# Kernel tuning notes

Hardware: AMD Instinct MI355X
Metric: run time of the kernel (lower is better)

The kernel has to match this reference:

```python
import jax, jax.numpy as jnp
import numpy as np

B, D, L = 4, 256, 4096

def setup_inputs() -> dict:
    key = jax.random.key(0)
    k1, k2, k3 = jax.random.split(key, 3)
    query = jax.random.normal(k1, (B, D, L), dtype=jnp.float32)
    context = jax.random.normal(k2, (B, D, L), dtype=jnp.float32)
    W_in = jax.random.normal(k3, (D, D), dtype=jnp.float32) * 0.02
    b_in = jnp.zeros((D,), dtype=jnp.float32)
    return {"query": query, "context": context, "W_in": W_in, "b_in": b_in}

def reference(query, context, W_in, b_in):
    # inputs are [B, D, L]; module transposes to [B, L, D]
    q = jnp.transpose(query, (0, 2, 1))    # [B, O, D]
    c = jnp.transpose(context, (0, 2, 1))  # [B, Q, D]
    # 'general': linear_in applied to query only (torch Linear: x @ W^T + b)
    q = q @ W_in.T + b_in
    # unscaled Luong attention: QK^T -> softmax -> A V
    scores = jnp.einsum('bod,bqd->boq', q, c)          # [B, O, Q]
    weights = jax.nn.softmax(scores, axis=-1)          # [B, O, Q]
    out = jnp.einsum('boq,bqd->bod', weights, c)       # [B, O, D]
    return (out, weights)
```

## Files before the change

kernel.cpp:

```cpp
#include <hip/hip_runtime.h>


#define BATCH 4
#define DDIM  256
#define LSEQ  4096
#define TQ    64

typedef float    f32x4 __attribute__((ext_vector_type(4)));
typedef _Float16 f16x8 __attribute__((ext_vector_type(8)));
typedef _Float16 f16x4 __attribute__((ext_vector_type(4)));

__device__ __forceinline__ void gld16(const void* g, void* l) {
  __builtin_amdgcn_global_load_lds((const __attribute__((address_space(1))) void*)g,
                                   (__attribute__((address_space(3))) void*)l, 16, 0, 0);
}

__global__ __launch_bounds__(256) void transpose_cast(
    const float* __restrict__ q_in, const float* __restrict__ c_in,
    _Float16* __restrict__ q_out, _Float16* __restrict__ c_out,
    _Float16* __restrict__ cD16)
{
  __shared__ float tile[64][68];
  const int which = blockIdx.z >> 2;
  const int b     = blockIdx.z & 3;
  const float* __restrict__ src = which ? c_in : q_in;
  _Float16* __restrict__ dst    = which ? c_out : q_out;
  const int l0 = blockIdx.x * 64, d0 = blockIdx.y * 64;
  const int tid = threadIdx.x;
  const int tr = tid >> 4, tc = (tid & 15) << 2;
#pragma unroll
  for (int i = 0; i < 4; ++i) {
    int d = tr + i * 16;
    f32x4 v = *(const f32x4*)(src + ((size_t)b * DDIM + d0 + d) * LSEQ + l0 + tc);
    *(f32x4*)&tile[d][tc] = v;
    if (which) {
      f16x4 h;
      h[0] = (_Float16)v[0]; h[1] = (_Float16)v[1];
      h[2] = (_Float16)v[2]; h[3] = (_Float16)v[3];
      *(f16x4*)(cD16 + ((size_t)b * DDIM + d0 + d) * LSEQ + l0 + tc) = h;
    }
  }
  __syncthreads();
#pragma unroll
  for (int i = 0; i < 4; ++i) {
    int l = tr + i * 16;
    f16x4 h;
    h[0] = (_Float16)tile[tc + 0][l];
    h[1] = (_Float16)tile[tc + 1][l];
    h[2] = (_Float16)tile[tc + 2][l];
    h[3] = (_Float16)tile[tc + 3][l];
    *(f16x4*)(dst + ((size_t)b * LSEQ + l0 + l) * DDIM + d0 + tc) = h;
  }
}

__global__ __launch_bounds__(256) void wconv(const float* __restrict__ w,
                                             _Float16* __restrict__ w16) {
  int i = (blockIdx.x * 256 + threadIdx.x) * 4;
  f32x4 v = *(const f32x4*)(w + i);
  f16x4 h;
  h[0] = (_Float16)v[0]; h[1] = (_Float16)v[1];
  h[2] = (_Float16)v[2]; h[3] = (_Float16)v[3];
  *(f16x4*)(w16 + i) = h;
}

__global__ __launch_bounds__(256) void linear_q(
    const _Float16* __restrict__ qT16, const _Float16* __restrict__ W16,
    const float* __restrict__ bias, _Float16* __restrict__ qw16)
{
  const int tid = threadIdx.x;
  const int wv = tid >> 6, ln = tid & 63, g = ln >> 4, c16 = ln & 15;
  const size_t r0 = (size_t)blockIdx.x * 64 + wv * 16;

  f16x8 qa[8];
  const _Float16* qrow = qT16 + (r0 + c16) * DDIM + g * 8;
#pragma unroll
  for (int kk = 0; kk < 8; ++kk) qa[kk] = *(const f16x8*)(qrow + kk * 32);

  f32x4 acc[16];
#pragma unroll
  for (int n = 0; n < 16; ++n) acc[n] = f32x4{0.f, 0.f, 0.f, 0.f};

#pragma unroll 2
  for (int kk = 0; kk < 8; ++kk) {
#pragma unroll
    for (int n = 0; n < 16; ++n) {
      f16x8 bf = *(const f16x8*)(W16 + (n * 16 + c16) * DDIM + kk * 32 + g * 8);
      acc[n] = __builtin_amdgcn_mfma_f32_16x16x32_f16(qa[kk], bf, acc[n], 0, 0, 0);
    }
  }
#pragma unroll
  for (int n = 0; n < 16; ++n) {
    float bb = bias[n * 16 + c16];
#pragma unroll
    for (int r = 0; r < 4; ++r)
      qw16[(r0 + 4 * g + r) * DDIM + n * 16 + c16] = (_Float16)(acc[n][r] + bb);
  }
}

__global__ __launch_bounds__(1024, 4) void attn_main(
    const _Float16* __restrict__ qw16,
    const _Float16* __restrict__ cT16,
    const _Float16* __restrict__ cD16,
    float* __restrict__ outp,
    float* __restrict__ wgt)
{
  __shared__ __align__(16) char smem[2][32768];
  __shared__ __align__(16) char wbuf[8192];
  __shared__ float redbuf[4][64];
  char* obuf = &smem[0][0];

  const int tid = threadIdx.x;
  const int wv  = tid >> 6;
  const int qw  = wv & 3;
  const int ow  = wv >> 2;
  const int kh  = wv & 1;
  const int dw  = wv >> 1;
  const int ln  = tid & 63;
  const int g   = ln >> 4;
  const int c16 = ln & 15;

  const int lin   = blockIdx.y * 64 + blockIdx.x;
  const int b     = (lin & 7) >> 1;
  const int otile = ((lin >> 3) << 1) | (lin & 1);
  const int o0    = otile * 64;
  const int bo    = b * LSEQ + o0;

  const _Float16* __restrict__ cbase = cT16 + (size_t)b * LSEQ * DDIM;
  const _Float16* __restrict__ cDb   = cD16 + (size_t)b * DDIM * LSEQ;

  f16x8 qb[8];
#pragma unroll
  for (int kk = 0; kk < 8; ++kk)
    qb[kk] = *(const f16x8*)(qw16 +
        ((size_t)(bo + ow * 16 + c16) << 8) + kk * 32 + g * 8);

  auto issue_dma = [&](int t, int pp) {
#pragma unroll
    for (int i = 0; i < 2; ++i) {
      unsigned x  = (unsigned)tid * 16 + i * 16384;
      unsigned q  = x >> 9;
      unsigned db = (x & 511u) ^ ((q & 7u) << 4);
      gld16(cbase + ((size_t)(t * TQ + q) << 8) + (db >> 1), &smem[pp][x]);
    }
  };

  float lsum = 0.f;
  int p = 0;
  issue_dma(0, 0);
  for (int t = 0; t < LSEQ / TQ; ++t) {
    asm volatile("s_waitcnt vmcnt(0)" ::: "memory");
    __builtin_amdgcn_s_barrier();
    issue_dma(t < LSEQ / TQ - 1 ? t + 1 : 0, p ^ 1);
    __builtin_amdgcn_sched_barrier(0);

    const char* cl = smem[p];
    f32x4 sa{0.f, 0.f, 0.f, 0.f};
#pragma unroll
    for (int kk = 0; kk < 8; ++kk) {
      unsigned off = (unsigned)((qw * 16 + c16) * 512 + kk * 64 + g * 16) ^
                     ((unsigned)(c16 & 7) << 4);
      f16x8 af = *(const f16x8*)(cl + off);
      sa = __builtin_amdgcn_mfma_f32_16x16x32_f16(af, qb[kk], sa, 0, 0, 0);
    }
#pragma unroll
    for (int r = 0; r < 4; ++r) lsum += __expf(sa[r]);
    p ^= 1;
  }

  lsum += __shfl_xor(lsum, 16);
  lsum += __shfl_xor(lsum, 32);
  if (ln < 16) redbuf[qw][ow * 16 + ln] = lsum;
  __syncthreads();
  const int o_mine = ow * 16 + c16;
  const float invl = 1.0f / (redbuf[0][o_mine] + redbuf[1][o_mine] +
                             redbuf[2][o_mine] + redbuf[3][o_mine]);

  f32x4 oacc[4][2];
#pragma unroll
  for (int m = 0; m < 4; ++m)
#pragma unroll
    for (int nf = 0; nf < 2; ++nf) oacc[m][nf] = f32x4{0.f, 0.f, 0.f, 0.f};

  for (int t = 0; t < LSEQ / TQ; ++t) {
    const int q0 = t * TQ;
    if (t == 0) asm volatile("s_waitcnt vmcnt(0)" ::: "memory");
    else        asm volatile("s_waitcnt vmcnt(1)" ::: "memory");
    __builtin_amdgcn_s_barrier();
    __builtin_amdgcn_sched_barrier(0);

    f16x8 bv[2];
#pragma unroll
    for (int nf = 0; nf < 2; ++nf)
      bv[nf] = *(const f16x8*)(cDb +
          ((size_t)(dw * 32 + nf * 16 + c16) << 12) + q0 + kh * 32 + g * 8);

    if (t < LSEQ / TQ - 1) issue_dma(t + 1, p ^ 1);

    const char* cl = smem[p];
    f32x4 sa{0.f, 0.f, 0.f, 0.f};
#pragma unroll
    for (int kk = 0; kk < 8; ++kk) {
      unsigned off = (unsigned)((qw * 16 + c16) * 512 + kk * 64 + g * 16) ^
                     ((unsigned)(c16 & 7) << 4);
      f16x8 af = *(const f16x8*)(cl + off);
      sa = __builtin_amdgcn_mfma_f32_16x16x32_f16(af, qb[kk], sa, 0, 0, 0);
    }

    {
      f32x4 wv4;
      f16x4 wh;
#pragma unroll
      for (int r = 0; r < 4; ++r) {
        float w = __expf(sa[r]) * invl;
        wv4[r] = w;
        wh[r]  = (_Float16)w;
      }
      *(f32x4*)(wgt + ((size_t)(bo + o_mine) << 12) + q0 + qw * 16 + 4 * g) = wv4;
      unsigned wb = (unsigned)(o_mine * 128 + (qw * 16 + 4 * g) * 2) ^
                    ((unsigned)(o_mine & 7) << 4);
      *(f16x4*)(wbuf + wb) = wh;
    }
    asm volatile("s_waitcnt lgkmcnt(0)" ::: "memory");
    __builtin_amdgcn_s_barrier();
    __builtin_amdgcn_sched_barrier(0);

#pragma unroll
    for (int m = 0; m < 4; ++m) {
      unsigned off = (unsigned)((m * 16 + c16) * 128 + kh * 64 + g * 16) ^
                     ((unsigned)(c16 & 7) << 4);
      f16x8 wa = *(const f16x8*)(wbuf + off);
#pragma unroll
      for (int nf = 0; nf < 2; ++nf)
        oacc[m][nf] =
            __builtin_amdgcn_mfma_f32_16x16x32_f16(wa, bv[nf], oacc[m][nf], 0, 0, 0);
    }
    p ^= 1;
  }

  __syncthreads();
  if (kh == 1) {
#pragma unroll
    for (int m = 0; m < 4; ++m)
#pragma unroll
      for (int nf = 0; nf < 2; ++nf)
        *(f32x4*)(obuf + dw * 8192 + (m * 2 + nf) * 1024 + ln * 16) = oacc[m][nf];
  }
  __syncthreads();
  if (kh == 0) {
#pragma unroll
    for (int m = 0; m < 4; ++m)
#pragma unroll
      for (int nf = 0; nf < 2; ++nf) {
        f32x4 o2 = *(const f32x4*)(obuf + dw * 8192 + (m * 2 + nf) * 1024 + ln * 16);
        f32x4 o  = oacc[m][nf] + o2;
#pragma unroll
        for (int r = 0; r < 4; ++r)
          outp[((size_t)(bo + m * 16 + 4 * g + r) << 8) + dw * 32 + nf * 16 + c16] = o[r];
      }
  }
}

extern "C" void kernel_launch(void* const* d_in, const int* in_sizes, int n_in,
                              void* d_out, int out_size, void* d_ws, size_t ws_size,
                              hipStream_t stream) {
  const float* query   = (const float*)d_in[0];
  const float* context = (const float*)d_in[1];
  const float* W_in    = (const float*)d_in[2];
  const float* b_in    = (const float*)d_in[3];

  float* outp = (float*)d_out;
  float* wgt  = outp + (size_t)BATCH * LSEQ * DDIM;

  const size_t NELEM = (size_t)BATCH * LSEQ * DDIM;
  _Float16* qT16 = (_Float16*)d_ws;
  _Float16* cT16 = qT16 + NELEM;
  _Float16* qw16 = cT16 + NELEM;
  _Float16* W16  = qw16 + NELEM;
  _Float16* cD16 = W16 + 65536;

  transpose_cast<<<dim3(LSEQ / 64, DDIM / 64, 2 * BATCH), 256, 0, stream>>>(
      query, context, qT16, cT16, cD16);
  wconv<<<(DDIM * DDIM) / 1024, 256, 0, stream>>>(W_in, W16);
  linear_q<<<(BATCH * LSEQ) / 64, 256, 0, stream>>>(qT16, W16, b_in, qw16);
  attn_main<<<dim3(64, BATCH), 1024, 0, stream>>>(qw16, cT16, cD16, outp, wgt);
}
```

Before: 266.7 us.

## Single-pass attention with deferred normalization via bf16 unnormalized weights

Removes the first scores pass that only computed softmax row sums. Scores are now computed once, exp values are stored unnormalized in bf16 both to a global scratch and to LDS for the AV MFMA (switched to bf16), and the row sums are accumulated alongside. Outputs are scaled by the inverse sum at the end, and a separate kernel expands the bf16 weights to fp32 with normalization. This halves the QK^T work but adds a 128MB bf16 write plus read, and loses precision in the weights output. It also assumes unscaled scores never overflow exp without max subtraction.

```diff
diff --git a/kernel.cpp b/kernel.cpp
--- a/kernel.cpp
+++ b/kernel.cpp
@@ -9,16 +9,24 @@
 typedef float    f32x4 __attribute__((ext_vector_type(4)));
 typedef _Float16 f16x8 __attribute__((ext_vector_type(8)));
 typedef _Float16 f16x4 __attribute__((ext_vector_type(4)));
+typedef short    b16x8 __attribute__((ext_vector_type(8)));
+typedef short    b16x4 __attribute__((ext_vector_type(4)));
+typedef unsigned short u16x8 __attribute__((ext_vector_type(8)));
 
 __device__ __forceinline__ void gld16(const void* g, void* l) {
   __builtin_amdgcn_global_load_lds((const __attribute__((address_space(1))) void*)g,
                                    (__attribute__((address_space(3))) void*)l, 16, 0, 0);
 }
 
+__device__ __forceinline__ short f2bf(float f) {
+  unsigned u = __builtin_bit_cast(unsigned, f);
+  return (short)((u + 0x7FFFu + ((u >> 16) & 1u)) >> 16);
+}
+
 __global__ __launch_bounds__(256) void transpose_cast(
     const float* __restrict__ q_in, const float* __restrict__ c_in,
     _Float16* __restrict__ q_out, _Float16* __restrict__ c_out,
-    _Float16* __restrict__ cD16)
+    short* __restrict__ cB16)
 {
   __shared__ float tile[64][68];
   const int which = blockIdx.z >> 2;
@@ -34,10 +42,10 @@
     f32x4 v = *(const f32x4*)(src + ((size_t)b * DDIM + d0 + d) * LSEQ + l0 + tc);
     *(f32x4*)&tile[d][tc] = v;
     if (which) {
-      f16x4 h;
-      h[0] = (_Float16)v[0]; h[1] = (_Float16)v[1];
-      h[2] = (_Float16)v[2]; h[3] = (_Float16)v[3];
-      *(f16x4*)(cD16 + ((size_t)b * DDIM + d0 + d) * LSEQ + l0 + tc) = h;
+      b16x4 h;
+      h[0] = f2bf(v[0]); h[1] = f2bf(v[1]);
+      h[2] = f2bf(v[2]); h[3] = f2bf(v[3]);
+      *(b16x4*)(cB16 + ((size_t)b * DDIM + d0 + d) * LSEQ + l0 + tc) = h;
     }
   }
   __syncthreads();
@@ -100,13 +108,15 @@
 __global__ __launch_bounds__(1024, 4) void attn_main(
     const _Float16* __restrict__ qw16,
     const _Float16* __restrict__ cT16,
-    const _Float16* __restrict__ cD16,
+    const short* __restrict__ cB16,
     float* __restrict__ outp,
-    float* __restrict__ wgt)
+    unsigned short* __restrict__ u16g,
+    float* __restrict__ invl_tab)
 {
   __shared__ __align__(16) char smem[2][32768];
   __shared__ __align__(16) char wbuf[8192];
   __shared__ float redbuf[4][64];
+  __shared__ float invbuf[64];
   char* obuf = &smem[0][0];
 
   const int tid = threadIdx.x;
@@ -126,7 +136,7 @@
   const int bo    = b * LSEQ + o0;
 
   const _Float16* __restrict__ cbase = cT16 + (size_t)b * LSEQ * DDIM;
-  const _Float16* __restrict__ cDb   = cD16 + (size_t)b * DDIM * LSEQ;
+  const short* __restrict__ cBb      = cB16 + (size_t)b * DDIM * LSEQ;
 
   f16x8 qb[8];
 #pragma unroll
@@ -144,16 +154,7 @@
     }
   };
 
-  float lsum = 0.f;
-  int p = 0;
-  issue_dma(0, 0);
-  for (int t = 0; t < LSEQ / TQ; ++t) {
-    asm volatile("s_waitcnt vmcnt(0)" ::: "memory");
-    __builtin_amdgcn_s_barrier();
-    issue_dma(t < LSEQ / TQ - 1 ? t + 1 : 0, p ^ 1);
-    __builtin_amdgcn_sched_barrier(0);
-
-    const char* cl = smem[p];
+  auto scores = [&](const char* cl) {
     f32x4 sa{0.f, 0.f, 0.f, 0.f};
 #pragma unroll
     for (int kk = 0; kk < 8; ++kk) {
@@ -162,25 +163,20 @@
       f16x8 af = *(const f16x8*)(cl + off);
       sa = __builtin_amdgcn_mfma_f32_16x16x32_f16(af, qb[kk], sa, 0, 0, 0);
     }
-#pragma unroll
-    for (int r = 0; r < 4; ++r) lsum += __expf(sa[r]);
-    p ^= 1;
-  }
-
-  lsum += __shfl_xor(lsum, 16);
-  lsum += __shfl_xor(lsum, 32);
-  if (ln < 16) redbuf[qw][ow * 16 + ln] = lsum;
-  __syncthreads();
+    return sa;
+  };
+
   const int o_mine = ow * 16 + c16;
-  const float invl = 1.0f / (redbuf[0][o_mine] + redbuf[1][o_mine] +
-                             redbuf[2][o_mine] + redbuf[3][o_mine]);
-
+
+  float ls = 0.f;
   f32x4 oacc[4][2];
 #pragma unroll
   for (int m = 0; m < 4; ++m)
 #pragma unroll
     for (int nf = 0; nf < 2; ++nf) oacc[m][nf] = f32x4{0.f, 0.f, 0.f, 0.f};
 
+  int p = 0;
+  issue_dma(0, 0);
   for (int t = 0; t < LSEQ / TQ; ++t) {
     const int q0 = t * TQ;
     if (t == 0) asm volatile("s_waitcnt vmcnt(0)" ::: "memory");
@@ -188,37 +184,29 @@
     __builtin_amdgcn_s_barrier();
     __builtin_amdgcn_sched_barrier(0);
 
-    f16x8 bv[2];
+    b16x8 bv[2];
 #pragma unroll
     for (int nf = 0; nf < 2; ++nf)
-      bv[nf] = *(const f16x8*)(cDb +
+      bv[nf] = *(const b16x8*)(cBb +
           ((size_t)(dw * 32 + nf * 16 + c16) << 12) + q0 + kh * 32 + g * 8);
 
     if (t < LSEQ / TQ - 1) issue_dma(t + 1, p ^ 1);
 
-    const char* cl = smem[p];
-    f32x4 sa{0.f, 0.f, 0.f, 0.f};
-#pragma unroll
-    for (int kk = 0; kk < 8; ++kk) {
-      unsigned off = (unsigned)((qw * 16 + c16) * 512 + kk * 64 + g * 16) ^
-                     ((unsigned)(c16 & 7) << 4);
-      f16x8 af = *(const f16x8*)(cl + off);
-      sa = __builtin_amdgcn_mfma_f32_16x16x32_f16(af, qb[kk], sa, 0, 0, 0);
-    }
+    f32x4 sa = scores(smem[p]);
 
     {
-      f32x4 wv4;
-      f16x4 wh;
+      b16x4 uh;
 #pragma unroll
       for (int r = 0; r < 4; ++r) {
-        float w = __expf(sa[r]) * invl;
-        wv4[r] = w;
-        wh[r]  = (_Float16)w;
+        float u = __expf(sa[r]);
+        ls += u;
+        uh[r] = f2bf(u);
       }
-      *(f32x4*)(wgt + ((size_t)(bo + o_mine) << 12) + q0 + qw * 16 + 4 * g) = wv4;
+      *(b16x4*)(u16g + ((size_t)(bo + o_mine) << 12) + q0 + qw * 16 + 4 * g) =
+          *(b16x4*)&uh;
       unsigned wb = (unsigned)(o_mine * 128 + (qw * 16 + 4 * g) * 2) ^
                     ((unsigned)(o_mine & 7) << 4);
-      *(f16x4*)(wbuf + wb) = wh;
+      *(b16x4*)(wbuf + wb) = uh;
     }
     asm volatile("s_waitcnt lgkmcnt(0)" ::: "memory");
     __builtin_amdgcn_s_barrier();
@@ -228,16 +216,27 @@
     for (int m = 0; m < 4; ++m) {
       unsigned off = (unsigned)((m * 16 + c16) * 128 + kh * 64 + g * 16) ^
                      ((unsigned)(c16 & 7) << 4);
-      f16x8 wa = *(const f16x8*)(wbuf + off);
+      b16x8 wa = *(const b16x8*)(wbuf + off);
 #pragma unroll
       for (int nf = 0; nf < 2; ++nf)
         oacc[m][nf] =
-            __builtin_amdgcn_mfma_f32_16x16x32_f16(wa, bv[nf], oacc[m][nf], 0, 0, 0);
+            __builtin_amdgcn_mfma_f32_16x16x32_bf16(wa, bv[nf], oacc[m][nf], 0, 0, 0);
     }
     p ^= 1;
   }
 
+  ls += __shfl_xor(ls, 16);
+  ls += __shfl_xor(ls, 32);
+  if (ln < 16) redbuf[qw][ow * 16 + ln] = ls;
   __syncthreads();
+  if (tid < 64) {
+    float s = redbuf[0][tid] + redbuf[1][tid] + redbuf[2][tid] + redbuf[3][tid];
+    float iv = 1.0f / s;
+    invbuf[tid] = iv;
+    invl_tab[bo + tid] = iv;
+  }
+  __syncthreads();
+
   if (kh == 1) {
 #pragma unroll
     for (int m = 0; m < 4; ++m)
@@ -254,9 +253,33 @@
         f32x4 o2 = *(const f32x4*)(obuf + dw * 8192 + (m * 2 + nf) * 1024 + ln * 16);
         f32x4 o  = oacc[m][nf] + o2;
 #pragma unroll
-        for (int r = 0; r < 4; ++r)
-          outp[((size_t)(bo + m * 16 + 4 * g + r) << 8) + dw * 32 + nf * 16 + c16] = o[r];
+        for (int r = 0; r < 4; ++r) {
+          float iv = invbuf[m * 16 + 4 * g + r];
+          outp[((size_t)(bo + m * 16 + 4 * g + r) << 8) + dw * 32 + nf * 16 + c16] =
+              o[r] * iv;
+        }
       }
+  }
+}
+
+__global__ __launch_bounds__(256) void normalize_w(
+    const unsigned short* __restrict__ u16g,
+    const float* __restrict__ invl_tab,
+    float* __restrict__ wgt)
+{
+  const size_t N = (size_t)BATCH * LSEQ * LSEQ;
+  const size_t stride = (size_t)gridDim.x * 256 * 8;
+  for (size_t i = ((size_t)blockIdx.x * 256 + threadIdx.x) * 8; i < N; i += stride) {
+    u16x8 v = *(const u16x8*)(u16g + i);
+    float iv = invl_tab[i >> 12];
+    f32x4 w0, w1;
+#pragma unroll
+    for (int j = 0; j < 4; ++j) {
+      w0[j] = __builtin_bit_cast(float, (unsigned)v[j] << 16) * iv;
+      w1[j] = __builtin_bit_cast(float, (unsigned)v[4 + j] << 16) * iv;
+    }
+    *(f32x4*)(wgt + i)     = w0;
+    *(f32x4*)(wgt + i + 4) = w1;
   }
 }
 
@@ -276,11 +299,15 @@
   _Float16* cT16 = qT16 + NELEM;
   _Float16* qw16 = cT16 + NELEM;
   _Float16* W16  = qw16 + NELEM;
-  _Float16* cD16 = W16 + 65536;
+  short*    cB16 = (short*)(W16 + 65536);
+  float*    invl_tab = (float*)(cB16 + NELEM);
+  unsigned short* u16g = (unsigned short*)(invl_tab + (size_t)BATCH * LSEQ);
 
   transpose_cast<<<dim3(LSEQ / 64, DDIM / 64, 2 * BATCH), 256, 0, stream>>>(
-      query, context, qT16, cT16, cD16);
+      query, context, qT16, cT16, cB16);
   wconv<<<(DDIM * DDIM) / 1024, 256, 0, stream>>>(W_in, W16);
   linear_q<<<(BATCH * LSEQ) / 64, 256, 0, stream>>>(qT16, W16, b_in, qw16);
-  attn_main<<<dim3(64, BATCH), 1024, 0, stream>>>(qw16, cT16, cD16, outp, wgt);
-}
+  attn_main<<<dim3(64, BATCH), 1024, 0, stream>>>(qw16, cT16, cB16, outp, u16g,
+                                                  invl_tab);
+  normalize_w<<<2048, 256, 0, stream>>>(u16g, invl_tab, wgt);
+}
```

Measured after the change: 292.5 us. 1.1x slower.
